# Optimization experiments

Hardware: AMD Instinct MI355X
Metric: run time of the kernel (lower is better)

Reference implementation:

```python
import jax, jax.numpy as jnp
import numpy as np

B, TQ, TKV, D_MODEL, H, DQ, DV = 4, 2048, 2048, 1024, 16, 64, 64
DK = DQ

def setup_inputs() -> dict:
    key = jax.random.key(0)
    ks = jax.random.split(key, 8)
    s = 0.02
    return {
        "query_sequence": jax.random.normal(ks[0], (B, TQ, D_MODEL), jnp.float32),
        "key_value_sequence": jax.random.normal(ks[1], (B, TKV, D_MODEL), jnp.float32),
        "key_value_padding_mask": jnp.zeros((B, TKV), dtype=bool),
        "Wq": jax.random.normal(ks[2], (D_MODEL, H * DQ), jnp.float32) * s,
        "bq": jnp.zeros((H * DQ,), jnp.float32),
        "Wkv": jax.random.normal(ks[3], (D_MODEL, H * (DK + DV)), jnp.float32) * s,
        "bkv": jnp.zeros((H * (DK + DV),), jnp.float32),
        "Wo": jax.random.normal(ks[4], (H * DV, D_MODEL), jnp.float32) * s,
        "bo": jnp.zeros((D_MODEL,), jnp.float32),
        "apply_causal_mask": 1,
    }

def reference(query_sequence, key_value_sequence, key_value_padding_mask,
              Wq, bq, Wkv, bkv, Wo, bo, apply_causal_mask):
    b, tq, _ = query_sequence.shape
    tkv = key_value_sequence.shape[1]
    q = (query_sequence @ Wq + bq).reshape(b, tq, H, DQ)          # (B,Tq,H,Dq)
    kv = key_value_sequence @ Wkv + bkv
    k = kv[..., : H * DK].reshape(b, tkv, H, DK)                   # (B,Tkv,H,Dk)
    v = kv[..., H * DK :].reshape(b, tkv, H, DV)                   # (B,Tkv,H,Dv)
    scores = jnp.einsum("bqhd,bkhd->bhqk", q, k) / jnp.sqrt(jnp.float32(DK))
    neg_inf = jnp.float32(-jnp.inf)
    scores = jnp.where(key_value_padding_mask[:, None, None, :], neg_inf, scores)
    if apply_causal_mask:
        causal = jnp.tril(jnp.ones((tq, tkv), dtype=bool))
        scores = jnp.where(causal[None, None, :, :], scores, neg_inf)
    attn = jax.nn.softmax(scores, axis=-1)
    out = jnp.einsum("bhqk,bkhd->bqhd", attn, v).reshape(b, tq, H * DV)
    return out @ Wo + bo
```

## Files before the change

### kernel.cpp

```cpp
#include <hip/hip_runtime.h>
#include <hip/hip_bf16.h>

#define B_   4
#define TQ_  2048
#define TKV_ 2048
#define DM_  1024
#define H_   16
#define DH_  64

#define SC_FOLD 0.18033688011112042f

using f32x4  = __attribute__((ext_vector_type(4))) float;
using f32x16 = __attribute__((ext_vector_type(16))) float;
using s16x8  = __attribute__((ext_vector_type(8))) short;

static __device__ __forceinline__ unsigned short f2bf(float f) {
  union { float f; unsigned int u; } v; v.f = f;
  unsigned int r = v.u + 0x7FFFu + ((v.u >> 16) & 1u);
  return (unsigned short)(r >> 16);
}
static __device__ __forceinline__ unsigned int pk2(float a, float b) {
  unsigned int r;
  asm("v_cvt_pk_bf16_f32 %0, %1, %2" : "=v"(r) : "v"(a), "v"(b));
  return r;
}
static __device__ __forceinline__ float max3f(float a, float b, float c) {
  float r;
  asm("v_max3_f32 %0, %1, %2, %3" : "=v"(r) : "v"(a), "v"(b), "v"(c));
  return r;
}

#define GL16(g, l)                                                          \
  __builtin_amdgcn_global_load_lds(                                         \
      (const __attribute__((address_space(1))) unsigned int*)(g),           \
      (__attribute__((address_space(3))) unsigned int*)(l), 16, 0, 0)

__global__ __launch_bounds__(256) void k_transpose_cast(
    const float* __restrict__ W, unsigned short* __restrict__ WT, int K, int N,
    float scale) {
  __shared__ float t[64][65];
  int n0 = blockIdx.x * 64, k0 = blockIdx.y * 64;
  int tx = threadIdx.x & 63, ty = threadIdx.x >> 6;
#pragma unroll
  for (int i = 0; i < 64; i += 4)
    t[ty + i][tx] = W[(size_t)(k0 + ty + i) * N + n0 + tx];
  __syncthreads();
#pragma unroll
  for (int i = 0; i < 64; i += 4)
    WT[(size_t)(n0 + ty + i) * K + k0 + tx] = f2bf(t[tx][ty + i] * scale);
}

__global__ __launch_bounds__(256) void k_cast_bf16(
    const float* __restrict__ in, unsigned short* __restrict__ out, int n4) {
  for (int i = blockIdx.x * 256 + threadIdx.x; i < n4; i += gridDim.x * 256) {
    f32x4 v = *(const f32x4*)(in + (size_t)i * 4);
    unsigned long long u = (unsigned long long)pk2(v[0], v[1]) |
                           ((unsigned long long)pk2(v[2], v[3]) << 32);
    *(unsigned long long*)(out + (size_t)i * 4) = u;
  }
}

template <int MODE, int BN>
__global__ __launch_bounds__(512, 2) void k_gemm8(
    const unsigned short* __restrict__ A, const unsigned short* __restrict__ BT,
    const float* __restrict__ bias, float bscale, unsigned short* __restrict__ out_a,
    unsigned short* __restrict__ out_b, float* __restrict__ out_f, int Kd) {
  constexpr int NI = BN / 64;
  constexpr int NH = NI / 2;
  __shared__ __align__(16) unsigned short As[2 * 256 * 64];
  __shared__ __align__(16) unsigned short Bs[2 * BN * 64];
  const int tid = threadIdx.x, lane = tid & 63, w = tid >> 6;
  const int wm = w >> 2, wn = w & 3;

  int nwg = gridDim.x * gridDim.y;
  int bid = blockIdx.y * gridDim.x + blockIdx.x;
  int cpx = nwg >> 3;
  int sw = (bid & 7) * cpx + (bid >> 3);
  int bx = sw % gridDim.x, by = sw / gridDim.x;
  int m0 = by * 256, n0 = bx * BN;

  const int strow = tid >> 3;
  const int sx = ((tid & 7) << 4) ^ ((strow & 7) << 4);
  const char* gA = (const char*)(A + (size_t)(m0 + strow) * Kd) + sx;
  const char* gB = (const char*)(BT + (size_t)(n0 + strow) * Kd) + sx;
  char* lA = (char*)As;
  char* lB = (char*)Bs;

#define ST_A(bf, c, k0) \
  GL16(gA + ((size_t)(c) * 64 * Kd + (size_t)(k0)) * 2, lA + (bf) * 32768 + (c) * 8192 + tid * 16)
#define ST_B(bf, c, k0) \
  GL16(gB + ((size_t)(c) * 64 * Kd + (size_t)(k0)) * 2, lB + (bf) * (BN * 128) + (c) * 8192 + tid * 16)

  f32x4 acc[8][NI];
#pragma unroll
  for (int i = 0; i < 8; ++i)
#pragma unroll
    for (int j = 0; j < NI; ++j) acc[i][j] = (f32x4){0.f, 0.f, 0.f, 0.f};

  s16x8 afr[4][2], bfr[NI][2];
  const int arow = wm * 128 + (lane & 15);
  const int brow = wn * (NI * 16) + (lane & 15);
  const int fcol = (lane >> 4) * 16;

#define RD_A(bf, r) (*(const s16x8*)(lA + (bf) * 32768 + (r) * 128 + ((fcol + _kk * 64) ^ (((r) & 7) << 4))))
#define RD_B(bf, r) (*(const s16x8*)(lB + (bf) * (BN * 128) + (r) * 128 + ((fcol + _kk * 64) ^ (((r) & 7) << 4))))

  const int nT = Kd >> 6;

  ST_B(0, 0, 0); ST_B(0, 1, 0);
  if (BN == 256) { ST_B(0, 2, 0); ST_B(0, 3, 0); }
  ST_A(0, 0, 0); ST_A(0, 2, 0);
  ST_A(0, 1, 0); ST_A(0, 3, 0);
  asm volatile("s_waitcnt vmcnt(2)" ::: "memory");
  __builtin_amdgcn_s_barrier();

#pragma unroll 1
  for (int t = 0; t < nT; ++t) {
    const int cur = t & 1, nxt = cur ^ 1;
    const int k1 = (t + 1) << 6;
    const bool st = (t + 1 < nT);

#pragma unroll
    for (int mi = 0; mi < 4; ++mi)
#pragma unroll
      for (int _kk = 0; _kk < 2; ++_kk) afr[mi][_kk] = RD_A(cur, arow + mi * 16);
#pragma unroll
    for (int ni = 0; ni < NH; ++ni)
#pragma unroll
      for (int _kk = 0; _kk < 2; ++_kk) bfr[ni][_kk] = RD_B(cur, brow + ni * 16);
    if (st) { ST_B(nxt, 0, k1); ST_B(nxt, 1, k1); }
    __builtin_amdgcn_s_barrier();
    __builtin_amdgcn_s_setprio(1);
#pragma unroll
    for (int mi = 0; mi < 4; ++mi)
#pragma unroll
      for (int ni = 0; ni < NH; ++ni)
#pragma unroll
        for (int kk = 0; kk < 2; ++kk)
          acc[mi][ni] = __builtin_amdgcn_mfma_f32_16x16x32_bf16(afr[mi][kk], bfr[ni][kk], acc[mi][ni], 0, 0, 0);
    __builtin_amdgcn_s_setprio(0);
    __builtin_amdgcn_s_barrier();

#pragma unroll
    for (int ni = NH; ni < NI; ++ni)
#pragma unroll
      for (int _kk = 0; _kk < 2; ++_kk) bfr[ni][_kk] = RD_B(cur, brow + ni * 16);
    if (st) {
      if (BN == 256) { ST_B(nxt, 2, k1); ST_B(nxt, 3, k1); }
      else           { ST_A(nxt, 0, k1); ST_A(nxt, 2, k1); }
    }
    if (st) asm volatile("s_waitcnt vmcnt(4)" ::: "memory");
    else    asm volatile("s_waitcnt vmcnt(0)" ::: "memory");
    __builtin_amdgcn_s_barrier();
    __builtin_amdgcn_s_setprio(1);
#pragma unroll
    for (int mi = 0; mi < 4; ++mi)
#pragma unroll
      for (int ni = NH; ni < NI; ++ni)
#pragma unroll
        for (int kk = 0; kk < 2; ++kk)
          acc[mi][ni] = __builtin_amdgcn_mfma_f32_16x16x32_bf16(afr[mi][kk], bfr[ni][kk], acc[mi][ni], 0, 0, 0);
    __builtin_amdgcn_s_setprio(0);
    __builtin_amdgcn_s_barrier();

#pragma unroll
    for (int mi = 0; mi < 4; ++mi)
#pragma unroll
      for (int _kk = 0; _kk < 2; ++_kk) afr[mi][_kk] = RD_A(cur, arow + (mi + 4) * 16);
    if (st) {
      if (BN == 256) { ST_A(nxt, 0, k1); ST_A(nxt, 2, k1); }
      else           { ST_A(nxt, 1, k1); ST_A(nxt, 3, k1); }
    }
    __builtin_amdgcn_s_barrier();
    __builtin_amdgcn_s_setprio(1);
#pragma unroll
    for (int mi = 0; mi < 4; ++mi)
#pragma unroll
      for (int ni = 0; ni < NH; ++ni)
#pragma unroll
        for (int kk = 0; kk < 2; ++kk)
          acc[mi + 4][ni] = __builtin_amdgcn_mfma_f32_16x16x32_bf16(afr[mi][kk], bfr[ni][kk], acc[mi + 4][ni], 0, 0, 0);
    __builtin_amdgcn_s_setprio(0);
    __builtin_amdgcn_s_barrier();

    if (st && BN == 256) { ST_A(nxt, 1, k1); ST_A(nxt, 3, k1); }
    asm volatile("s_waitcnt vmcnt(2)" ::: "memory");
    __builtin_amdgcn_s_barrier();
    __builtin_amdgcn_s_setprio(1);
#pragma unroll
    for (int mi = 0; mi < 4; ++mi)
#pragma unroll
      for (int ni = NH; ni < NI; ++ni)
#pragma unroll
        for (int kk = 0; kk < 2; ++kk)
          acc[mi + 4][ni] = __builtin_amdgcn_mfma_f32_16x16x32_bf16(afr[mi][kk], bfr[ni][kk], acc[mi + 4][ni], 0, 0, 0);
    __builtin_amdgcn_s_setprio(0);
    __builtin_amdgcn_s_barrier();
  }

#pragma unroll
  for (int mi = 0; mi < 8; ++mi) {
#pragma unroll
    for (int ni = 0; ni < NI; ++ni) {
      int col = n0 + wn * (NI * 16) + ni * 16 + (lane & 15);
      int rbase = m0 + wm * 128 + mi * 16 + (lane >> 4) * 4;
      float bv = bias[col] * bscale;
      if (MODE == 1 && col >= H_ * DH_) {
        int c2 = col - H_ * DH_;
        int h = c2 >> 6, d = c2 & 63;
        int b = rbase >> 11, tt = rbase & 2047;
        union { unsigned short h4[4]; unsigned long long u; } p;
#pragma unroll
        for (int r = 0; r < 4; ++r) p.h4[r] = f2bf(acc[mi][ni][r] + bv);
        *(unsigned long long*)(out_b + ((((size_t)b * H_ + h) * DH_ + d) * TKV_ + tt)) = p.u;
      } else {
#pragma unroll
        for (int r = 0; r < 4; ++r) {
          float v = acc[mi][ni][r] + bv;
          int m = rbase + r;
          if (MODE == 0) {
            int b = m >> 11, tt = m & 2047;
            int h = col >> 6, d = col & 63;
            out_a[(((size_t)b * H_ + h) * TQ_ + tt) * DH_ + d] = f2bf(v);
          } else if (MODE == 1) {
            int b = m >> 11, tt = m & 2047;
            int h = col >> 6, d = col & 63;
            out_a[(((size_t)b * H_ + h) * TKV_ + tt) * DH_ + d] = f2bf(v);
          } else {
            out_f[(size_t)m * DM_ + col] = v;
          }
        }
      }
    }
  }
#undef ST_A
#undef ST_B
#undef RD_A
#undef RD_B
}

__global__ __launch_bounds__(256, 3) void k_attn(
    const unsigned short* __restrict__ Qb, const unsigned short* __restrict__ Kb,
    const unsigned short* __restrict__ Vtb, const unsigned char* __restrict__ mask,
    const int* __restrict__ cflag, unsigned short* __restrict__ Ob) {
  __shared__ __align__(16) unsigned short Kt[64 * 64];
  __shared__ __align__(16) unsigned short Vt[64 * 64];
  __shared__ float bias_lds[64];
  __shared__ float red[4][32];
  __shared__ int s_any;

  int bid = blockIdx.y * gridDim.x + blockIdx.x;
  int r8 = bid & 7, q8 = bid >> 3;
  int bh = r8 * 8 + (q8 >> 3);
  int bx = q8 & 7;

  int b = bh >> 4, h = bh & 15;
  int tid = threadIdx.x, lane = tid & 63, w = tid >> 6;
  int hi = lane >> 5, l31 = lane & 31, l7 = lane & 7;
  const unsigned short* Qp = Qb + (size_t)bh * TQ_ * DH_;
  const char* Kp = (const char*)(Kb + (size_t)bh * TKV_ * DH_);
  const char* Vp = (const char*)(Vtb + (size_t)bh * DH_ * TKV_);
  const unsigned char* mp = mask + (size_t)b * TKV_;
  int causal = cflag[0];
  char* kbase = (char*)Kt;
  char* vbase = (char*)Vt;

  int st_row = tid >> 2;
  int st_cb0 = (tid & 3) * 16;
  s16x8 pKr[2], pVr[2];

#define LOAD_KV(kv0)                                                          \
  {                                                                           \
    _Pragma("unroll")                                                         \
    for (int p = 0; p < 2; ++p) {                                             \
      int cb = st_cb0 + p * 64;                                               \
      pKr[p] = *(const s16x8*)(Kp + ((size_t)((kv0) + st_row) * 128 + cb));   \
      pVr[p] = *(const s16x8*)(Vp + (((size_t)st_row * TKV_ + (kv0)) * 2 + cb)); \
    }                                                                         \
  }
#define WRITE_KV()                                                            \
  {                                                                           \
    _Pragma("unroll")                                                         \
    for (int p = 0; p < 2; ++p) {                                             \
      int cb = st_cb0 + p * 64;                                               \
      int sw = cb ^ ((st_row & 7) << 4);                                      \
      *(s16x8*)(kbase + st_row * 128 + sw) = pKr[p];                          \
      *(s16x8*)(vbase + st_row * 128 + sw) = pVr[p];                          \
    }                                                                         \
  }

  if (tid == 0) s_any = 0;
  __syncthreads();
  {
    int any = 0;
    for (int i = tid; i < TKV_; i += 256) any |= mp[i];
    if (any) s_any = 1;
  }
  __syncthreads();
  const int has_mask = s_any;

#pragma unroll 1
  for (int pass = 0; pass < 2; ++pass) {
    int qb = (pass ? (15 - bx) : bx) * 128;
    int qw = qb + w * 32;
    int qrow = qw + l31;

    s16x8 bQ[4];
#pragma unroll
    for (int kk = 0; kk < 4; ++kk)
      bQ[kk] = *(const s16x8*)(Qp + (size_t)qrow * DH_ + kk * 16 + hi * 8);

    f32x16 accO[2];
#pragma unroll
    for (int i = 0; i < 16; ++i) { accO[0][i] = 0.f; accO[1][i] = 0.f; }
    float m_run = -INFINITY, l_run = 0.f;

    int nT = (causal ? (qb + 128) : TKV_) >> 6;

    LOAD_KV(0);
    WRITE_KV();
    if (has_mask && tid < 64) bias_lds[tid] = mp[tid] ? -1e30f : 0.0f;
    __syncthreads();

#pragma unroll 1
    for (int it = 0; it < nT; ++it) {
      int kv0 = it << 6;
      if (it + 1 < nT) LOAD_KV(kv0 + 64);

      if (!(causal && kv0 >= qw + 32)) {
        f32x16 sT[2];
#pragma unroll
        for (int i = 0; i < 16; ++i) { sT[0][i] = 0.f; sT[1][i] = 0.f; }
        __builtin_amdgcn_s_setprio(1);
#pragma unroll
        for (int s = 0; s < 2; ++s) {
#pragma unroll
          for (int kk = 0; kk < 4; ++kk) {
            s16x8 aK = *(const s16x8*)(kbase + (s * 32 + l31) * 128 +
                                       ((kk * 32 + hi * 16) ^ (l7 << 4)));
            sT[s] = __builtin_amdgcn_mfma_f32_32x32x16_bf16(aK, bQ[kk], sT[s], 0, 0, 0);
          }
        }
        __builtin_amdgcn_s_setprio(0);

        int diag = causal && (kv0 + 64 > qw);
        float a0, a1, a2, a3;
        if (diag || has_mask) {
#pragma unroll
          for (int s = 0; s < 2; ++s)
#pragma unroll
            for (int r = 0; r < 16; ++r) {
              int kvloc = s * 32 + (r & 3) + 8 * (r >> 2) + 4 * hi;
              float sv = sT[s][r];
              if (has_mask) sv += bias_lds[kvloc];
              if (diag && (kv0 + kvloc) > qrow) sv = -1e30f;
              sT[s][r] = sv;
            }
        }
        a0 = sT[0][0]; a1 = sT[0][1]; a2 = sT[0][2]; a3 = sT[0][3];
#pragma unroll
        for (int r = 4; r < 16; r += 4) {
          a0 = fmaxf(a0, sT[0][r + 0]); a1 = fmaxf(a1, sT[0][r + 1]);
          a2 = fmaxf(a2, sT[0][r + 2]); a3 = fmaxf(a3, sT[0][r + 3]);
        }
#pragma unroll
        for (int r = 0; r < 16; r += 4) {
          a0 = fmaxf(a0, sT[1][r + 0]); a1 = fmaxf(a1, sT[1][r + 1]);
          a2 = fmaxf(a2, sT[1][r + 2]); a3 = fmaxf(a3, sT[1][r + 3]);
        }
        float mx = max3f(max3f(a0, a1, a2), a3, -3.0e30f);
        mx = fmaxf(mx, __shfl_xor(mx, 32));

        if (!__all(mx - m_run <= 8.0f)) {
          float mnew = fmaxf(m_run, mx);
          float sc_o = exp2f(m_run - mnew);
          m_run = mnew;
          l_run *= sc_o;
          red[w][l31] = sc_o;
#pragma unroll
          for (int r = 0; r < 16; ++r) {
            float f = red[w][(r & 3) + 8 * (r >> 2) + 4 * hi];
            accO[0][r] *= f;
            accO[1][r] *= f;
          }
        }

        float s0acc = 0.f, s1acc = 0.f, s2acc = 0.f, s3acc = 0.f;
#pragma unroll
        for (int s = 0; s < 2; ++s)
#pragma unroll
          for (int r = 0; r < 16; r += 4) {
            float p0 = exp2f(sT[s][r + 0] - m_run);
            float p1 = exp2f(sT[s][r + 1] - m_run);
            float p2 = exp2f(sT[s][r + 2] - m_run);
            float p3 = exp2f(sT[s][r + 3] - m_run);
            sT[s][r + 0] = p0; sT[s][r + 1] = p1;
            sT[s][r + 2] = p2; sT[s][r + 3] = p3;
            s0acc += p0; s1acc += p1; s2acc += p2; s3acc += p3;
          }
        float ls = (s0acc + s1acc) + (s2acc + s3acc);
        ls += __shfl_xor(ls, 32);
        l_run += ls;

#pragma unroll
        for (int c = 0; c < 4; ++c) {
          int s = c >> 1, kk = c & 1;
          unsigned int x0 = pk2(sT[s][8 * kk + 0], sT[s][8 * kk + 1]);
          unsigned int y0 = pk2(sT[s][8 * kk + 2], sT[s][8 * kk + 3]);
          unsigned int x1 = pk2(sT[s][8 * kk + 4], sT[s][8 * kk + 5]);
          unsigned int y1 = pk2(sT[s][8 * kk + 6], sT[s][8 * kk + 7]);
          unsigned int sx0 = __shfl_xor(x0, 32), sy0 = __shfl_xor(y0, 32);
          unsigned int sx1 = __shfl_xor(x1, 32), sy1 = __shfl_xor(y1, 32);
          union { unsigned int u[4]; s16x8 v; } pf;
          pf.u[0] = hi ? sx1 : x0;
          pf.u[1] = hi ? sy1 : y0;
          pf.u[2] = hi ? x1 : sx0;
          pf.u[3] = hi ? y1 : sy0;
          __builtin_amdgcn_s_setprio(1);
#pragma unroll
          for (int dt = 0; dt < 2; ++dt) {
            s16x8 vf = *(const s16x8*)(vbase + (dt * 32 + l31) * 128 +
                                       ((c * 32 + hi * 16) ^ (l7 << 4)));
            accO[dt] = __builtin_amdgcn_mfma_f32_32x32x16_bf16(pf.v, vf, accO[dt], 0, 0, 0);
          }
          __builtin_amdgcn_s_setprio(0);
        }
      }

      __syncthreads();
      if (it + 1 < nT) {
        WRITE_KV();
        if (has_mask && tid < 64) bias_lds[tid] = mp[kv0 + 64 + tid] ? -1e30f : 0.0f;
      }
      __syncthreads();
    }

    red[w][l31] = 1.0f / l_run;
#pragma unroll
    for (int r = 0; r < 16; ++r) {
      int R = (r & 3) + 8 * (r >> 2) + 4 * hi;
      float f = red[w][R];
      int qg = qw + R;
      size_t base = ((size_t)b * TQ_ + qg) * DM_ + h * DH_ + l31;
      Ob[base] = f2bf(accO[0][r] * f);
      Ob[base + 32] = f2bf(accO[1][r] * f);
    }
  }
#undef LOAD_KV
#undef WRITE_KV
}

extern "C" void kernel_launch(void* const* d_in, const int* in_sizes, int n_in,
                              void* d_out, int out_size, void* d_ws, size_t ws_size,
                              hipStream_t stream) {
  const float* xq  = (const float*)d_in[0];
  const float* xkv = (const float*)d_in[1];
  const unsigned char* mask = (const unsigned char*)d_in[2];
  const float* Wq  = (const float*)d_in[3];
  const float* bq  = (const float*)d_in[4];
  const float* Wkv = (const float*)d_in[5];
  const float* bkv = (const float*)d_in[6];
  const float* Wo  = (const float*)d_in[7];
  const float* bo  = (const float*)d_in[8];
  const int* cflag = (const int*)d_in[9];
  float* out = (float*)d_out;

  char* ws = (char*)d_ws;
  unsigned short* WqT  = (unsigned short*)(ws);
  unsigned short* WkvT = (unsigned short*)(ws + ((size_t)2 << 20));
  unsigned short* WoT  = (unsigned short*)(ws + ((size_t)6 << 20));
  unsigned short* Qb   = (unsigned short*)(ws + ((size_t)8 << 20));
  unsigned short* Kb   = (unsigned short*)(ws + ((size_t)24 << 20));
  unsigned short* Vb   = (unsigned short*)(ws + ((size_t)40 << 20));
  unsigned short* Xr   = (unsigned short*)(ws + ((size_t)56 << 20));
  unsigned short* Ob   = Xr;

  k_transpose_cast<<<dim3(16, 16), 256, 0, stream>>>(Wq, WqT, 1024, 1024, SC_FOLD);
  k_transpose_cast<<<dim3(32, 16), 256, 0, stream>>>(Wkv, WkvT, 1024, 2048, 1.0f);
  k_transpose_cast<<<dim3(16, 16), 256, 0, stream>>>(Wo, WoT, 1024, 1024, 1.0f);

  k_cast_bf16<<<2048, 256, 0, stream>>>(xq, Xr, B_ * TQ_ * DM_ / 4);
  k_gemm8<0, 128><<<dim3(8, 32), 512, 0, stream>>>(Xr, WqT, bq, SC_FOLD, Qb, nullptr, nullptr, 1024);

  k_cast_bf16<<<2048, 256, 0, stream>>>(xkv, Xr, B_ * TKV_ * DM_ / 4);
  k_gemm8<1, 256><<<dim3(8, 32), 512, 0, stream>>>(Xr, WkvT, bkv, 1.0f, Kb, Vb, nullptr, 1024);

  k_attn<<<dim3(8, B_ * H_), 256, 0, stream>>>(Qb, Kb, Vb, mask, cflag, Ob);

  k_gemm8<2, 128><<<dim3(8, 32), 512, 0, stream>>>(Ob, WoT, bo, 1.0f, nullptr, nullptr, out, 1024);
}
```

Before: 207.9 us.

## Widen attention KV tile to 128 keys with per-subtile causal skipping

Doubles the KV tile staged in shared memory per iteration from 64 to 128 keys, halving the number of loop iterations and the barriers between them. Each wave now computes up to four 32-key score subtiles, and only those not fully masked by causality are processed. Shared-memory and register use grow, so launch bounds drop from 3 to 2 blocks per CU, which reduces occupancy. The V swizzle in the XOR pattern now uses a 256-byte row stride, and the bank-conflict behaviour of that layout may change.

```diff
diff --git a/kernel.cpp b/kernel.cpp
--- a/kernel.cpp
+++ b/kernel.cpp
@@ -239,13 +239,13 @@
 #undef RD_B
 }
 
-__global__ __launch_bounds__(256, 3) void k_attn(
+__global__ __launch_bounds__(256, 2) void k_attn(
     const unsigned short* __restrict__ Qb, const unsigned short* __restrict__ Kb,
     const unsigned short* __restrict__ Vtb, const unsigned char* __restrict__ mask,
     const int* __restrict__ cflag, unsigned short* __restrict__ Ob) {
-  __shared__ __align__(16) unsigned short Kt[64 * 64];
-  __shared__ __align__(16) unsigned short Vt[64 * 64];
-  __shared__ float bias_lds[64];
+  __shared__ __align__(16) unsigned short Kt[128 * 64];
+  __shared__ __align__(16) unsigned short Vt[64 * 128];
+  __shared__ float bias_lds[128];
   __shared__ float red[4][32];
   __shared__ int s_any;
 
@@ -265,27 +265,30 @@
   char* kbase = (char*)Kt;
   char* vbase = (char*)Vt;
 
-  int st_row = tid >> 2;
-  int st_cb0 = (tid & 3) * 16;
-  s16x8 pKr[2], pVr[2];
+  int st_r4 = tid >> 2;
+  int st_c4 = (tid & 3) * 16;
+  s16x8 pKr[4], pVr[4];
 
 #define LOAD_KV(kv0)                                                          \
   {                                                                           \
     _Pragma("unroll")                                                         \
-    for (int p = 0; p < 2; ++p) {                                             \
-      int cb = st_cb0 + p * 64;                                               \
-      pKr[p] = *(const s16x8*)(Kp + ((size_t)((kv0) + st_row) * 128 + cb));   \
-      pVr[p] = *(const s16x8*)(Vp + (((size_t)st_row * TKV_ + (kv0)) * 2 + cb)); \
+    for (int p = 0; p < 4; ++p) {                                             \
+      int krow = (p >> 1) * 64 + st_r4;                                       \
+      int kx = st_c4 + (p & 1) * 64;                                          \
+      pKr[p] = *(const s16x8*)(Kp + ((size_t)((kv0) + krow) * 128 + kx));     \
+      int vx = st_c4 + p * 64;                                                \
+      pVr[p] = *(const s16x8*)(Vp + (((size_t)st_r4 * TKV_ + (kv0)) * 2 + vx)); \
     }                                                                         \
   }
 #define WRITE_KV()                                                            \
   {                                                                           \
     _Pragma("unroll")                                                         \
-    for (int p = 0; p < 2; ++p) {                                             \
-      int cb = st_cb0 + p * 64;                                               \
-      int sw = cb ^ ((st_row & 7) << 4);                                      \
-      *(s16x8*)(kbase + st_row * 128 + sw) = pKr[p];                          \
-      *(s16x8*)(vbase + st_row * 128 + sw) = pVr[p];                          \
+    for (int p = 0; p < 4; ++p) {                                             \
+      int krow = (p >> 1) * 64 + st_r4;                                       \
+      int kx = st_c4 + (p & 1) * 64;                                          \
+      *(s16x8*)(kbase + krow * 128 + (kx ^ ((st_r4 & 7) << 4))) = pKr[p];     \
+      int vx = st_c4 + p * 64;                                                \
+      *(s16x8*)(vbase + st_r4 * 256 + (vx ^ ((st_r4 & 7) << 4))) = pVr[p];    \
     }                                                                         \
   }
 
@@ -315,58 +318,64 @@
     for (int i = 0; i < 16; ++i) { accO[0][i] = 0.f; accO[1][i] = 0.f; }
     float m_run = -INFINITY, l_run = 0.f;
 
-    int nT = (causal ? (qb + 128) : TKV_) >> 6;
+    int nT = (causal ? (qb + 128) : TKV_) >> 7;
 
     LOAD_KV(0);
     WRITE_KV();
-    if (has_mask && tid < 64) bias_lds[tid] = mp[tid] ? -1e30f : 0.0f;
+    if (has_mask && tid < 128) bias_lds[tid] = mp[tid] ? -1e30f : 0.0f;
     __syncthreads();
 
 #pragma unroll 1
     for (int it = 0; it < nT; ++it) {
-      int kv0 = it << 6;
-      if (it + 1 < nT) LOAD_KV(kv0 + 64);
-
-      if (!(causal && kv0 >= qw + 32)) {
-        f32x16 sT[2];
-#pragma unroll
-        for (int i = 0; i < 16; ++i) { sT[0][i] = 0.f; sT[1][i] = 0.f; }
+      int kv0 = it << 7;
+      if (it + 1 < nT) LOAD_KV(kv0 + 128);
+
+      int nact = 4;
+      if (causal) {
+        int rem = qw + 31 - kv0;
+        nact = rem < 0 ? 0 : ((rem >> 5) + 1);
+        if (nact > 4) nact = 4;
+      }
+
+      if (nact > 0) {
+        f32x16 sT[4];
         __builtin_amdgcn_s_setprio(1);
 #pragma unroll
-        for (int s = 0; s < 2; ++s) {
-#pragma unroll
-          for (int kk = 0; kk < 4; ++kk) {
-            s16x8 aK = *(const s16x8*)(kbase + (s * 32 + l31) * 128 +
-                                       ((kk * 32 + hi * 16) ^ (l7 << 4)));
-            sT[s] = __builtin_amdgcn_mfma_f32_32x32x16_bf16(aK, bQ[kk], sT[s], 0, 0, 0);
+        for (int s = 0; s < 4; ++s) {
+          if (s < nact) {
+#pragma unroll
+            for (int i = 0; i < 16; ++i) sT[s][i] = 0.f;
+#pragma unroll
+            for (int kk = 0; kk < 4; ++kk) {
+              s16x8 aK = *(const s16x8*)(kbase + (s * 32 + l31) * 128 +
+                                         ((kk * 32 + hi * 16) ^ (l7 << 4)));
+              sT[s] = __builtin_amdgcn_mfma_f32_32x32x16_bf16(aK, bQ[kk], sT[s], 0, 0, 0);
+            }
           }
         }
         __builtin_amdgcn_s_setprio(0);
 
-        int diag = causal && (kv0 + 64 > qw);
-        float a0, a1, a2, a3;
-        if (diag || has_mask) {
-#pragma unroll
-          for (int s = 0; s < 2; ++s)
-#pragma unroll
-            for (int r = 0; r < 16; ++r) {
-              int kvloc = s * 32 + (r & 3) + 8 * (r >> 2) + 4 * hi;
-              float sv = sT[s][r];
-              if (has_mask) sv += bias_lds[kvloc];
-              if (diag && (kv0 + kvloc) > qrow) sv = -1e30f;
-              sT[s][r] = sv;
+        float a0 = -INFINITY, a1 = -INFINITY, a2 = -INFINITY, a3 = -INFINITY;
+#pragma unroll
+        for (int s = 0; s < 4; ++s) {
+          if (s < nact) {
+            int diag_s = causal && (kv0 + s * 32 + 31 > qw);
+            if (diag_s || has_mask) {
+#pragma unroll
+              for (int r = 0; r < 16; ++r) {
+                int kvloc = s * 32 + (r & 3) + 8 * (r >> 2) + 4 * hi;
+                float sv = sT[s][r];
+                if (has_mask) sv += bias_lds[kvloc];
+                if (diag_s && (kv0 + kvloc) > qrow) sv = -1e30f;
+                sT[s][r] = sv;
+              }
             }
-        }
-        a0 = sT[0][0]; a1 = sT[0][1]; a2 = sT[0][2]; a3 = sT[0][3];
-#pragma unroll
-        for (int r = 4; r < 16; r += 4) {
-          a0 = fmaxf(a0, sT[0][r + 0]); a1 = fmaxf(a1, sT[0][r + 1]);
-          a2 = fmaxf(a2, sT[0][r + 2]); a3 = fmaxf(a3, sT[0][r + 3]);
-        }
-#pragma unroll
-        for (int r = 0; r < 16; r += 4) {
-          a0 = fmaxf(a0, sT[1][r + 0]); a1 = fmaxf(a1, sT[1][r + 1]);
-          a2 = fmaxf(a2, sT[1][r + 2]); a3 = fmaxf(a3, sT[1][r + 3]);
+#pragma unroll
+            for (int r = 0; r < 16; r += 4) {
+              a0 = fmaxf(a0, sT[s][r + 0]); a1 = fmaxf(a1, sT[s][r + 1]);
+              a2 = fmaxf(a2, sT[s][r + 2]); a3 = fmaxf(a3, sT[s][r + 3]);
+            }
+          }
         }
         float mx = max3f(max3f(a0, a1, a2), a3, -3.0e30f);
         mx = fmaxf(mx, __shfl_xor(mx, 32));
@@ -387,50 +396,55 @@
 
         float s0acc = 0.f, s1acc = 0.f, s2acc = 0.f, s3acc = 0.f;
 #pragma unroll
-        for (int s = 0; s < 2; ++s)
-#pragma unroll
-          for (int r = 0; r < 16; r += 4) {
-            float p0 = exp2f(sT[s][r + 0] - m_run);
-            float p1 = exp2f(sT[s][r + 1] - m_run);
-            float p2 = exp2f(sT[s][r + 2] - m_run);
-            float p3 = exp2f(sT[s][r + 3] - m_run);
-            sT[s][r + 0] = p0; sT[s][r + 1] = p1;
-            sT[s][r + 2] = p2; sT[s][r + 3] = p3;
-            s0acc += p0; s1acc += p1; s2acc += p2; s3acc += p3;
+        for (int s = 0; s < 4; ++s) {
+          if (s < nact) {
+#pragma unroll
+            for (int r = 0; r < 16; r += 4) {
+              float p0 = exp2f(sT[s][r + 0] - m_run);
+              float p1 = exp2f(sT[s][r + 1] - m_run);
+              float p2 = exp2f(sT[s][r + 2] - m_run);
+              float p3 = exp2f(sT[s][r + 3] - m_run);
+              sT[s][r + 0] = p0; sT[s][r + 1] = p1;
+              sT[s][r + 2] = p2; sT[s][r + 3] = p3;
+              s0acc += p0; s1acc += p1; s2acc += p2; s3acc += p3;
+            }
           }
+        }
         float ls = (s0acc + s1acc) + (s2acc + s3acc);
         ls += __shfl_xor(ls, 32);
         l_run += ls;
 
 #pragma unroll
-        for (int c = 0; c < 4; ++c) {
-          int s = c >> 1, kk = c & 1;
-          unsigned int x0 = pk2(sT[s][8 * kk + 0], sT[s][8 * kk + 1]);
-          unsigned int y0 = pk2(sT[s][8 * kk + 2], sT[s][8 * kk + 3]);
-          unsigned int x1 = pk2(sT[s][8 * kk + 4], sT[s][8 * kk + 5]);
-          unsigned int y1 = pk2(sT[s][8 * kk + 6], sT[s][8 * kk + 7]);
-          unsigned int sx0 = __shfl_xor(x0, 32), sy0 = __shfl_xor(y0, 32);
-          unsigned int sx1 = __shfl_xor(x1, 32), sy1 = __shfl_xor(y1, 32);
-          union { unsigned int u[4]; s16x8 v; } pf;
-          pf.u[0] = hi ? sx1 : x0;
-          pf.u[1] = hi ? sy1 : y0;
-          pf.u[2] = hi ? x1 : sx0;
-          pf.u[3] = hi ? y1 : sy0;
-          __builtin_amdgcn_s_setprio(1);
-#pragma unroll
-          for (int dt = 0; dt < 2; ++dt) {
-            s16x8 vf = *(const s16x8*)(vbase + (dt * 32 + l31) * 128 +
-                                       ((c * 32 + hi * 16) ^ (l7 << 4)));
-            accO[dt] = __builtin_amdgcn_mfma_f32_32x32x16_bf16(pf.v, vf, accO[dt], 0, 0, 0);
+        for (int c = 0; c < 8; ++c) {
+          if ((c >> 1) < nact) {
+            int s = c >> 1, kk = c & 1;
+            unsigned int x0 = pk2(sT[s][8 * kk + 0], sT[s][8 * kk + 1]);
+            unsigned int y0 = pk2(sT[s][8 * kk + 2], sT[s][8 * kk + 3]);
+            unsigned int x1 = pk2(sT[s][8 * kk + 4], sT[s][8 * kk + 5]);
+            unsigned int y1 = pk2(sT[s][8 * kk + 6], sT[s][8 * kk + 7]);
+            unsigned int sx0 = __shfl_xor(x0, 32), sy0 = __shfl_xor(y0, 32);
+            unsigned int sx1 = __shfl_xor(x1, 32), sy1 = __shfl_xor(y1, 32);
+            union { unsigned int u[4]; s16x8 v; } pf;
+            pf.u[0] = hi ? sx1 : x0;
+            pf.u[1] = hi ? sy1 : y0;
+            pf.u[2] = hi ? x1 : sx0;
+            pf.u[3] = hi ? y1 : sy0;
+            __builtin_amdgcn_s_setprio(1);
+#pragma unroll
+            for (int dt = 0; dt < 2; ++dt) {
+              s16x8 vf = *(const s16x8*)(vbase + (dt * 32 + l31) * 256 +
+                                         ((c * 32 + hi * 16) ^ (l7 << 4)));
+              accO[dt] = __builtin_amdgcn_mfma_f32_32x32x16_bf16(pf.v, vf, accO[dt], 0, 0, 0);
+            }
+            __builtin_amdgcn_s_setprio(0);
           }
-          __builtin_amdgcn_s_setprio(0);
         }
       }
 
       __syncthreads();
       if (it + 1 < nT) {
         WRITE_KV();
-        if (has_mask && tid < 64) bias_lds[tid] = mp[kv0 + 64 + tid] ? -1e30f : 0.0f;
+        if (has_mask && tid < 128) bias_lds[tid] = mp[kv0 + 128 + tid] ? -1e30f : 0.0f;
       }
       __syncthreads();
     }
```

Measured after the change: 200.5 us. 3.6% less time.
